# Kernel optimization log

Measured on AMD Instinct MI355X. Metric: run time of the kernel, lower is better.

Reference implementation:

```python
import jax, jax.numpy as jnp
import numpy as np

B, I, H = 512, 256, 512
UNFOLDS = 6


def setup_inputs() -> dict:
    key = jax.random.key(0)
    ks = jax.random.split(key, 13)
    u = lambda k, shape, lo, hi: jax.random.uniform(k, shape, jnp.float32, lo, hi)
    sensory_erev = (2.0 * jax.random.randint(ks[3], (I, H), 0, 2) - 1.0).astype(jnp.float32)
    erev = (2.0 * jax.random.randint(ks[7], (H, H), 0, 2) - 1.0).astype(jnp.float32)
    return {
        "inputs": jax.random.normal(ks[0], (B, I), jnp.float32),
        "state": jax.random.normal(ks[1], (B, H), jnp.float32),
        "sensory_mu": u(ks[2], (I, H), 0.3, 0.8),
        "sensory_sigma": u(ks[4], (I, H), 3.0, 8.0),
        "sensory_W": u(ks[5], (I, H), 0.01, 1.0),
        "sensory_erev": sensory_erev,
        "mu": u(ks[6], (H, H), 0.3, 0.8),
        "sigma": u(ks[8], (H, H), 3.0, 8.0),
        "W": u(ks[9], (H, H), 0.01, 1.0),
        "erev": erev,
        "vleak": u(ks[10], (H,), -0.2, 0.2),
        "gleak": jnp.ones((H,), jnp.float32),
        "cm": jnp.full((H,), 0.5, jnp.float32),
    }


def reference(inputs, state, sensory_mu, sensory_sigma, sensory_W, sensory_erev,
              mu, sigma, W, erev, vleak, gleak, cm):
    # Sensory synapse currents (computed once): (B, I, H) broadcast
    sensory_act = jax.nn.sigmoid((inputs[:, :, None] - sensory_mu[None]) * sensory_sigma[None])
    sensory_w_act = sensory_W[None] * sensory_act                      # (B, I, H)
    w_num_sensory = jnp.sum(sensory_w_act * sensory_erev[None], axis=1)  # (B, H)
    w_den_sensory = jnp.sum(sensory_w_act, axis=1)                        # (B, H)

    def step(v_pre, _):
        # recurrent synapse gating: (B, H_pre, H_post)
        act = jax.nn.sigmoid((v_pre[:, :, None] - mu[None]) * sigma[None])
        w_act = W[None] * act
        w_num = jnp.sum(w_act * erev[None], axis=1) + w_num_sensory
        w_den = jnp.sum(w_act, axis=1) + w_den_sensory
        numerator = cm * v_pre + gleak * vleak + w_num
        denominator = cm + gleak + w_den
        return numerator / (denominator + 1e-8), None

    v_pre, _ = jax.lax.scan(step, state, None, length=UNFOLDS)
    return v_pre
```

## Files before the change

### kernel.cpp

```cpp
#include <hip/hip_runtime.h>

#define LTC_B 512
#define LTC_H 512
#define LTC_I 256

static constexpr float kL2E = 1.4426950408889634f;

template<int K, int LOG2K>
__global__ void ltc_prep(const float* __restrict__ mu, const float* __restrict__ sigma,
                         const float* __restrict__ W, const float* __restrict__ erev,
                         float4* __restrict__ slab) {
    const int t = blockIdx.x * 256 + threadIdx.x;
    if (t >= K * LTC_H) return;
    const int hh4  = t & 3;
    const int rest = t >> 2;
    const int j    = rest & (K - 1);
    const int ht4  = rest >> LOG2K;
    const int h    = ht4 * 4 + hh4;
    const int g    = j * LTC_H + h;
    const float sg = sigma[g];
    float4 o;
    o.x = -sg * kL2E;
    o.y = exp2f(mu[g] * sg * kL2E);
    o.z = W[g] * erev[g];
    o.w = W[g];
    slab[t] = o;
}

__global__ void ltc_transpose(const float* __restrict__ in, float* __restrict__ out,
                              int R, int C) {
    __shared__ float tile[64][65];
    const int bx = blockIdx.x * 64;
    const int by = blockIdx.y * 64;
    const int tx = threadIdx.x & 63;
    const int t4 = threadIdx.x >> 6;
    #pragma unroll
    for (int r = t4; r < 64; r += 4)
        tile[r][tx] = in[(size_t)(by + r) * C + bx + tx];
    __syncthreads();
    #pragma unroll
    for (int r = t4; r < 64; r += 4)
        out[(size_t)(bx + r) * R + by + tx] = tile[tx][r];
}

template<int K, int MODE>
__global__ __launch_bounds__(512, 8)
void ltc_pass(const float* __restrict__ vT,
              const float4* __restrict__ slab,
              const float* __restrict__ snumT, const float* __restrict__ sdenT,
              const float* __restrict__ vleak, const float* __restrict__ gleak,
              const float* __restrict__ cm,
              float* __restrict__ o0, float* __restrict__ o1)
{
    constexpr int JW = K / 8;
    __shared__ float2 comb[8][4][64];

    const int tid  = threadIdx.x;
    const int lane = tid & 63;
    const int wu   = __builtin_amdgcn_readfirstlane(tid >> 6);
    const int ht4  = blockIdx.x;
    const int b0   = blockIdx.y * 64;

    const float4* __restrict__ wq = slab + ((size_t)ht4 * K + wu * JW) * 4;
    const float*  __restrict__ vp = vT + (size_t)(wu * JW) * LTC_B + b0 + lane;

    float na0 = 0.f, da0 = 0.f, na1 = 0.f, da1 = 0.f;
    float na2 = 0.f, da2 = 0.f, na3 = 0.f, da3 = 0.f;

    #pragma unroll 4
    for (int jj = 0; jj < JW; ++jj) {
        const float vj = vp[(size_t)jj * LTC_B];
        const float4 q0 = wq[jj * 4 + 0];
        const float4 q1 = wq[jj * 4 + 1];
        const float4 q2 = wq[jj * 4 + 2];
        const float4 q3 = wq[jj * 4 + 3];
        const float e0 = __builtin_amdgcn_exp2f(q0.x * vj);
        const float e1 = __builtin_amdgcn_exp2f(q1.x * vj);
        const float e2 = __builtin_amdgcn_exp2f(q2.x * vj);
        const float e3 = __builtin_amdgcn_exp2f(q3.x * vj);
        const float d0 = fmaf(q0.y, e0, 1.0f);
        const float d1 = fmaf(q1.y, e1, 1.0f);
        const float d2 = fmaf(q2.y, e2, 1.0f);
        const float d3 = fmaf(q3.y, e3, 1.0f);
        const float r01 = __builtin_amdgcn_rcpf(d0 * d1);
        const float r23 = __builtin_amdgcn_rcpf(d2 * d3);
        const float s0 = r01 * d1, s1 = r01 * d0;
        const float s2 = r23 * d3, s3 = r23 * d2;
        na0 = fmaf(q0.z, s0, na0); da0 = fmaf(q0.w, s0, da0);
        na1 = fmaf(q1.z, s1, na1); da1 = fmaf(q1.w, s1, da1);
        na2 = fmaf(q2.z, s2, na2); da2 = fmaf(q2.w, s2, da2);
        na3 = fmaf(q3.z, s3, na3); da3 = fmaf(q3.w, s3, da3);
    }

    comb[wu][0][lane] = make_float2(na0, da0);
    comb[wu][1][lane] = make_float2(na1, da1);
    comb[wu][2][lane] = make_float2(na2, da2);
    comb[wu][3][lane] = make_float2(na3, da3);
    __syncthreads();

    if (wu < 4) {
        float na = 0.f, da = 0.f;
        #pragma unroll
        for (int js = 0; js < 8; ++js) {
            const float2 p = comb[js][wu][lane];
            na += p.x; da += p.y;
        }
        const int h = ht4 * 4 + wu;
        const int b = b0 + lane;
        const size_t hb = (size_t)h * LTC_B + b;
        if constexpr (MODE == 0) {
            o0[hb] = na;
            o1[hb] = da;
        } else {
            const float gl = gleak[h], vl = vleak[h], c0 = cm[h];
            const float vpre = vT[hb];
            const float num = fmaf(c0, vpre, gl * vl) + na + snumT[hb];
            const float den = c0 + gl + da + sdenT[hb];
            const float vn = num * __builtin_amdgcn_rcpf(den + 1e-8f);
            if constexpr (MODE == 1) o0[hb] = vn;
            else o0[(size_t)b * LTC_H + h] = vn;
        }
    }
}

extern "C" void kernel_launch(void* const* d_in, const int* in_sizes, int n_in,
                              void* d_out, int out_size, void* d_ws, size_t ws_size,
                              hipStream_t stream) {
    const float* inputs = (const float*)d_in[0];
    const float* state  = (const float*)d_in[1];
    const float* smu    = (const float*)d_in[2];
    const float* ssig   = (const float*)d_in[3];
    const float* sW     = (const float*)d_in[4];
    const float* serev  = (const float*)d_in[5];
    const float* mu     = (const float*)d_in[6];
    const float* sig    = (const float*)d_in[7];
    const float* W      = (const float*)d_in[8];
    const float* erev   = (const float*)d_in[9];
    const float* vleak  = (const float*)d_in[10];
    const float* gleak  = (const float*)d_in[11];
    const float* cm     = (const float*)d_in[12];

    float* out = (float*)d_out;
    char*  ws  = (char*)d_ws;
    float*  snumT = (float*)(ws);
    float*  sdenT = (float*)(ws + 1 * 1048576);
    float*  vTA   = (float*)(ws + 2 * 1048576);
    float*  vTB   = (float*)(ws + 3 * 1048576);
    float4* rslab = (float4*)(ws + 4 * 1048576);
    float4* sslab = (float4*)(ws + 8 * 1048576);
    float*  inpT  = (float*)(ws + 10 * 1048576);

    ltc_prep<LTC_H, 9><<<LTC_H * LTC_H / 256, 256, 0, stream>>>(mu, sig, W, erev, rslab);
    ltc_prep<LTC_I, 8><<<LTC_I * LTC_H / 256, 256, 0, stream>>>(smu, ssig, sW, serev, sslab);

    ltc_transpose<<<dim3(LTC_I / 64, LTC_B / 64), 256, 0, stream>>>(inputs, inpT, LTC_B, LTC_I);
    ltc_transpose<<<dim3(LTC_H / 64, LTC_B / 64), 256, 0, stream>>>(state, vTA, LTC_B, LTC_H);

    dim3 grid(LTC_H / 4, LTC_B / 64);
    dim3 blk(512);

    ltc_pass<LTC_I, 0><<<grid, blk, 0, stream>>>(
        inpT, sslab, nullptr, nullptr, nullptr, nullptr, nullptr, snumT, sdenT);

    const float* vin = vTA;
    float* vping[5] = {vTB, vTA, vTB, vTA, vTB};
    for (int s = 0; s < 5; ++s) {
        ltc_pass<LTC_H, 1><<<grid, blk, 0, stream>>>(
            vin, rslab, snumT, sdenT, vleak, gleak, cm, vping[s], nullptr);
        vin = vping[s];
    }
    ltc_pass<LTC_H, 2><<<grid, blk, 0, stream>>>(
        vin, rslab, snumT, sdenT, vleak, gleak, cm, out, nullptr);
}
```

Before: 291.5 us.

## Double-buffer weight slab via global_load_lds and store state in float4-interleaved layout

```diff
diff --git a/kernel.cpp b/kernel.cpp
--- a/kernel.cpp
+++ b/kernel.cpp
@@ -5,6 +5,14 @@
 #define LTC_I 256
 
 static constexpr float kL2E = 1.4426950408889634f;
+
+typedef unsigned int u32;
+#define AS_G __attribute__((address_space(1)))
+#define AS_L __attribute__((address_space(3)))
+
+__device__ __forceinline__ void ldg_lds16(const void* g, void* l) {
+    __builtin_amdgcn_global_load_lds((const AS_G u32*)g, (AS_L u32*)l, 16, 0, 0);
+}
 
 template<int K, int LOG2K>
 __global__ void ltc_prep(const float* __restrict__ mu, const float* __restrict__ sigma,
@@ -27,8 +35,8 @@
     slab[t] = o;
 }
 
-__global__ void ltc_transpose(const float* __restrict__ in, float* __restrict__ out,
-                              int R, int C) {
+__global__ void ltc_transpose_v4(const float* __restrict__ in, float* __restrict__ out,
+                                 int R, int C) {
     __shared__ float tile[64][65];
     const int bx = blockIdx.x * 64;
     const int by = blockIdx.y * 64;
@@ -39,13 +47,15 @@
         tile[r][tx] = in[(size_t)(by + r) * C + bx + tx];
     __syncthreads();
     #pragma unroll
-    for (int r = t4; r < 64; r += 4)
-        out[(size_t)(bx + r) * R + by + tx] = tile[tx][r];
+    for (int c = t4; c < 64; c += 4) {
+        const int k = bx + c;
+        out[((size_t)(k >> 2) * R + by + tx) * 4 + (k & 3)] = tile[tx][c];
+    }
 }
 
 template<int K, int MODE>
 __global__ __launch_bounds__(512, 8)
-void ltc_pass(const float* __restrict__ vT,
+void ltc_pass(const float4* __restrict__ vT4,
               const float4* __restrict__ slab,
               const float* __restrict__ snumT, const float* __restrict__ sdenT,
               const float* __restrict__ vleak, const float* __restrict__ gleak,
@@ -53,6 +63,9 @@
               float* __restrict__ o0, float* __restrict__ o1)
 {
     constexpr int JW = K / 8;
+    constexpr int NW = JW / 16;
+
+    __shared__ float4 wbuf[8][2][64];
     __shared__ float2 comb[8][4][64];
 
     const int tid  = threadIdx.x;
@@ -61,35 +74,54 @@
     const int ht4  = blockIdx.x;
     const int b0   = blockIdx.y * 64;
 
-    const float4* __restrict__ wq = slab + ((size_t)ht4 * K + wu * JW) * 4;
-    const float*  __restrict__ vp = vT + (size_t)(wu * JW) * LTC_B + b0 + lane;
+    const char* sbase = (const char*)slab + ((size_t)ht4 * K + (size_t)wu * JW) * 64;
+    const float4* __restrict__ vp4 = vT4 + (size_t)(wu * (JW / 4)) * LTC_B + b0 + lane;
 
     float na0 = 0.f, da0 = 0.f, na1 = 0.f, da1 = 0.f;
     float na2 = 0.f, da2 = 0.f, na3 = 0.f, da3 = 0.f;
-
-    #pragma unroll 4
-    for (int jj = 0; jj < JW; ++jj) {
-        const float vj = vp[(size_t)jj * LTC_B];
-        const float4 q0 = wq[jj * 4 + 0];
-        const float4 q1 = wq[jj * 4 + 1];
-        const float4 q2 = wq[jj * 4 + 2];
-        const float4 q3 = wq[jj * 4 + 3];
-        const float e0 = __builtin_amdgcn_exp2f(q0.x * vj);
-        const float e1 = __builtin_amdgcn_exp2f(q1.x * vj);
-        const float e2 = __builtin_amdgcn_exp2f(q2.x * vj);
-        const float e3 = __builtin_amdgcn_exp2f(q3.x * vj);
-        const float d0 = fmaf(q0.y, e0, 1.0f);
-        const float d1 = fmaf(q1.y, e1, 1.0f);
-        const float d2 = fmaf(q2.y, e2, 1.0f);
-        const float d3 = fmaf(q3.y, e3, 1.0f);
-        const float r01 = __builtin_amdgcn_rcpf(d0 * d1);
-        const float r23 = __builtin_amdgcn_rcpf(d2 * d3);
-        const float s0 = r01 * d1, s1 = r01 * d0;
-        const float s2 = r23 * d3, s3 = r23 * d2;
-        na0 = fmaf(q0.z, s0, na0); da0 = fmaf(q0.w, s0, da0);
-        na1 = fmaf(q1.z, s1, na1); da1 = fmaf(q1.w, s1, da1);
-        na2 = fmaf(q2.z, s2, na2); da2 = fmaf(q2.w, s2, da2);
-        na3 = fmaf(q3.z, s3, na3); da3 = fmaf(q3.w, s3, da3);
+    float4 vbuf[2][4];
+
+    ldg_lds16(sbase + (size_t)lane * 16, &wbuf[wu][0][0]);
+    #pragma unroll
+    for (int q = 0; q < 4; ++q) vbuf[0][q] = vp4[(size_t)q * LTC_B];
+
+    #pragma unroll
+    for (int w = 0; w < NW; ++w) {
+        asm volatile("s_waitcnt vmcnt(0) lgkmcnt(0)" ::: "memory");
+        if (w + 1 < NW) {
+            ldg_lds16(sbase + (w + 1) * 1024 + (size_t)lane * 16,
+                      &wbuf[wu][(w + 1) & 1][0]);
+            #pragma unroll
+            for (int q = 0; q < 4; ++q)
+                vbuf[(w + 1) & 1][q] = vp4[(size_t)((w + 1) * 4 + q) * LTC_B];
+        }
+        const float4* wq = &wbuf[wu][w & 1][0];
+        #pragma unroll
+        for (int jl = 0; jl < 16; ++jl) {
+            const float4 vv = vbuf[w & 1][jl >> 2];
+            const float vj = (jl & 3) == 0 ? vv.x : (jl & 3) == 1 ? vv.y
+                           : (jl & 3) == 2 ? vv.z : vv.w;
+            const float4 q0 = wq[jl * 4 + 0];
+            const float4 q1 = wq[jl * 4 + 1];
+            const float4 q2 = wq[jl * 4 + 2];
+            const float4 q3 = wq[jl * 4 + 3];
+            const float e0 = __builtin_amdgcn_exp2f(q0.x * vj);
+            const float e1 = __builtin_amdgcn_exp2f(q1.x * vj);
+            const float e2 = __builtin_amdgcn_exp2f(q2.x * vj);
+            const float e3 = __builtin_amdgcn_exp2f(q3.x * vj);
+            const float d0 = fmaf(q0.y, e0, 1.0f);
+            const float d1 = fmaf(q1.y, e1, 1.0f);
+            const float d2 = fmaf(q2.y, e2, 1.0f);
+            const float d3 = fmaf(q3.y, e3, 1.0f);
+            const float r01 = __builtin_amdgcn_rcpf(d0 * d1);
+            const float r23 = __builtin_amdgcn_rcpf(d2 * d3);
+            const float s0 = r01 * d1, s1 = r01 * d0;
+            const float s2 = r23 * d3, s3 = r23 * d2;
+            na0 = fmaf(q0.z, s0, na0); da0 = fmaf(q0.w, s0, da0);
+            na1 = fmaf(q1.z, s1, na1); da1 = fmaf(q1.w, s1, da1);
+            na2 = fmaf(q2.z, s2, na2); da2 = fmaf(q2.w, s2, da2);
+            na3 = fmaf(q3.z, s3, na3); da3 = fmaf(q3.w, s3, da3);
+        }
     }
 
     comb[wu][0][lane] = make_float2(na0, da0);
@@ -107,17 +139,19 @@
         }
         const int h = ht4 * 4 + wu;
         const int b = b0 + lane;
-        const size_t hb = (size_t)h * LTC_B + b;
         if constexpr (MODE == 0) {
+            const size_t hb = (size_t)h * LTC_B + b;
             o0[hb] = na;
             o1[hb] = da;
         } else {
+            const size_t hb = (size_t)h * LTC_B + b;
+            const size_t v4i = ((size_t)ht4 * LTC_B + b) * 4 + wu;
             const float gl = gleak[h], vl = vleak[h], c0 = cm[h];
-            const float vpre = vT[hb];
+            const float vpre = ((const float*)vT4)[v4i];
             const float num = fmaf(c0, vpre, gl * vl) + na + snumT[hb];
             const float den = c0 + gl + da + sdenT[hb];
             const float vn = num * __builtin_amdgcn_rcpf(den + 1e-8f);
-            if constexpr (MODE == 1) o0[hb] = vn;
+            if constexpr (MODE == 1) o0[v4i] = vn;
             else o0[(size_t)b * LTC_H + h] = vn;
         }
     }
@@ -144,29 +178,30 @@
     char*  ws  = (char*)d_ws;
     float*  snumT = (float*)(ws);
     float*  sdenT = (float*)(ws + 1 * 1048576);
-    float*  vTA   = (float*)(ws + 2 * 1048576);
-    float*  vTB   = (float*)(ws + 3 * 1048576);
+    float4* vA    = (float4*)(ws + 2 * 1048576);
+    float4* vB    = (float4*)(ws + 3 * 1048576);
     float4* rslab = (float4*)(ws + 4 * 1048576);
     float4* sslab = (float4*)(ws + 8 * 1048576);
-    float*  inpT  = (float*)(ws + 10 * 1048576);
+    float4* inpT4 = (float4*)(ws + 10 * 1048576);
 
     ltc_prep<LTC_H, 9><<<LTC_H * LTC_H / 256, 256, 0, stream>>>(mu, sig, W, erev, rslab);
     ltc_prep<LTC_I, 8><<<LTC_I * LTC_H / 256, 256, 0, stream>>>(smu, ssig, sW, serev, sslab);
 
-    ltc_transpose<<<dim3(LTC_I / 64, LTC_B / 64), 256, 0, stream>>>(inputs, inpT, LTC_B, LTC_I);
-    ltc_transpose<<<dim3(LTC_H / 64, LTC_B / 64), 256, 0, stream>>>(state, vTA, LTC_B, LTC_H);
+    ltc_transpose_v4<<<dim3(LTC_I / 64, LTC_B / 64), 256, 0, stream>>>(inputs, (float*)inpT4, LTC_B, LTC_I);
+    ltc_transpose_v4<<<dim3(LTC_H / 64, LTC_B / 64), 256, 0, stream>>>(state, (float*)vA, LTC_B, LTC_H);
 
     dim3 grid(LTC_H / 4, LTC_B / 64);
     dim3 blk(512);
 
     ltc_pass<LTC_I, 0><<<grid, blk, 0, stream>>>(
-        inpT, sslab, nullptr, nullptr, nullptr, nullptr, nullptr, snumT, sdenT);
-
-    const float* vin = vTA;
-    float* vping[5] = {vTB, vTA, vTB, vTA, vTB};
+        inpT4, sslab, nullptr, nullptr, nullptr, nullptr, nullptr,
+        (float*)snumT, (float*)sdenT);
+
+    const float4* vin = vA;
+    float4* vping[5] = {vB, vA, vB, vA, vB};
     for (int s = 0; s < 5; ++s) {
         ltc_pass<LTC_H, 1><<<grid, blk, 0, stream>>>(
-            vin, rslab, snumT, sdenT, vleak, gleak, cm, vping[s], nullptr);
+            vin, rslab, snumT, sdenT, vleak, gleak, cm, (float*)vping[s], nullptr);
         vin = vping[s];
     }
     ltc_pass<LTC_H, 2><<<grid, blk, 0, stream>>>(
```

New measurement: 397.7 us. 1.36x slower.
